# Kernel tuning notes

Measured on AMD Instinct MI355X. Metric: run time of the kernel, lower is better.

Reference implementation:

```python
import jax, jax.numpy as jnp
import numpy as np

N = 50000      # nodes
E = 1600000    # edges (avg degree 32)
R = 32         # num_rels
B = 8          # num_bases
DIN = 128
DOUT = 128


def setup_inputs() -> dict:
    key = jax.random.key(0)
    ks = jax.random.split(key, 7)
    x = jax.random.normal(ks[0], (N, DIN), dtype=jnp.float32)
    src = jax.random.randint(ks[1], (E,), 0, N, dtype=jnp.int32)
    dst = jax.random.randint(ks[2], (E,), 0, N, dtype=jnp.int32)
    etypes = jax.random.randint(ks[3], (E,), 0, R, dtype=jnp.int32)
    weight = jax.random.normal(ks[4], (B, DIN, DOUT), dtype=jnp.float32) * 0.05
    w_comp = jax.random.normal(ks[5], (R, B), dtype=jnp.float32) * 0.3
    h_bias = jnp.zeros((DOUT,), dtype=jnp.float32)
    loop_weight = jax.random.normal(ks[6], (DIN, DOUT), dtype=jnp.float32) * 0.05
    return {"x": x, "src": src, "dst": dst, "etypes": etypes,
            "weight": weight, "w_comp": w_comp, "h_bias": h_bias,
            "loop_weight": loop_weight}


def reference(x, src, dst, etypes, weight, w_comp, h_bias, loop_weight):
    # RelGraphConv, basis regularizer, self_loop=True, bias=True, act=relu, eval (dropout=0).
    # Message m_e = h_{src_e} @ W_{etype_e}, with W_r = sum_b w_comp[r,b] * weight[b].
    # Aggregation is sum over in-edges; since messages are linear in h_src we
    # segment-sum sources into (dst, relation) buckets first, then apply W_r once
    # per node -- identical math, no per-edge [Din,Dout] weight materialization.
    n = x.shape[0]
    r = w_comp.shape[0]
    seg = dst.astype(jnp.int32) * r + etypes.astype(jnp.int32)        # [E]
    agg = jax.ops.segment_sum(x[src], seg, num_segments=n * r)        # [N*R, Din]
    agg = agg.reshape(n, r, -1)                                       # [N, R, Din]
    tmp = jnp.einsum('nri,rb->nbi', agg, w_comp)                      # fold relations into bases
    h = jnp.einsum('nbi,bio->no', tmp, weight)                        # [N, Dout]
    h = h + h_bias + x @ loop_weight                                  # bias + self-loop
    return jax.nn.relu(h)
```

## Files before the change

kernel.cpp:

```cpp
#include <hip/hip_runtime.h>

#define N_NODES 50000
#define N_EDGES 1600000
#define NREL 32
#define NBASES 8
#define DIN 128
#define DOUT 128
#define KTOT (NBASES * DIN)
#define KSL (KTOT + DIN)
#define NODES_PER_BLOCK 8


__global__ void k_hist(const int* __restrict__ dst, int* __restrict__ deg) {
    int e = blockIdx.x * blockDim.x + threadIdx.x;
    if (e < N_EDGES) atomicAdd(&deg[dst[e]], 1);
}

__global__ void k_scan(const int* __restrict__ deg, int* __restrict__ indptr) {
    __shared__ int sdata[1024];
    const int T = 1024;
    int t = threadIdx.x;
    const int chunk = (N_NODES + T - 1) / T;
    int lo = t * chunk;
    int hi = lo + chunk; if (hi > N_NODES) hi = N_NODES;
    if (lo > N_NODES) lo = N_NODES;
    int s = 0;
    for (int i = lo; i < hi; ++i) s += deg[i];
    sdata[t] = s;
    __syncthreads();
    for (int off = 1; off < T; off <<= 1) {
        int v = (t >= off) ? sdata[t - off] : 0;
        __syncthreads();
        sdata[t] += v;
        __syncthreads();
    }
    int base = (t == 0) ? 0 : sdata[t - 1];
    for (int i = lo; i < hi; ++i) { indptr[i] = base; base += deg[i]; }
    if (t == T - 1) indptr[N_NODES] = sdata[T - 1];
}

__global__ void k_scatter(const int* __restrict__ dst,
                          const int* __restrict__ src,
                          const int* __restrict__ ety,
                          const int* __restrict__ indptr,
                          int* __restrict__ cursor,
                          int* __restrict__ packed) {
    int e = blockIdx.x * blockDim.x + threadIdx.x;
    if (e < N_EDGES) {
        int d = dst[e];
        int pos = atomicAdd(&cursor[d], 1);
        packed[indptr[d] + pos] = src[e] | (ety[e] << 16);
    }
}


#define EDGE_FMA(P, XV)                                                      \
    do {                                                                     \
        const float4 wA_ = *(const float4*)&wc[((P) >> 16) * NBASES];        \
        const float4 wB_ = *(const float4*)&wc[((P) >> 16) * NBASES + 4];    \
        a0x += wA_.x * (XV).x; a0y += wA_.x * (XV).y;                        \
        a1x += wA_.y * (XV).x; a1y += wA_.y * (XV).y;                        \
        a2x += wA_.z * (XV).x; a2y += wA_.z * (XV).y;                        \
        a3x += wA_.w * (XV).x; a3y += wA_.w * (XV).y;                        \
        a4x += wB_.x * (XV).x; a4y += wB_.x * (XV).y;                        \
        a5x += wB_.y * (XV).x; a5y += wB_.y * (XV).y;                        \
        a6x += wB_.z * (XV).x; a6y += wB_.z * (XV).y;                        \
        a7x += wB_.w * (XV).x; a7y += wB_.w * (XV).y;                        \
    } while (0)

__launch_bounds__(256, 2)
__global__ void k_fused(const float* __restrict__ x,
                        const float* __restrict__ weight,
                        const float* __restrict__ w_comp,
                        const float* __restrict__ h_bias,
                        const float* __restrict__ loop_w,
                        const int* __restrict__ indptr,
                        const int* __restrict__ packed,
                        float* __restrict__ out) {
    __shared__ __align__(16) float wc[NREL * NBASES];
    __shared__ __align__(16) float tmp[NODES_PER_BLOCK][KSL];

    const int tid  = threadIdx.x;
    const int lane = tid & 63;
    const int wid  = tid >> 6;
    const int nbase = blockIdx.x * NODES_PER_BLOCK;

    wc[tid & 255] = w_comp[tid & 255];
    __syncthreads();

    for (int rep = 0; rep < 2; ++rep) {
        const int nl = wid + rep * 4;
        const int node = nbase + nl;
        float a0x = 0.f, a0y = 0.f, a1x = 0.f, a1y = 0.f;
        float a2x = 0.f, a2y = 0.f, a3x = 0.f, a3y = 0.f;
        float a4x = 0.f, a4y = 0.f, a5x = 0.f, a5y = 0.f;
        float a6x = 0.f, a6y = 0.f, a7x = 0.f, a7y = 0.f;

        *(float2*)&tmp[nl][KTOT + 2 * lane] =
            *(const float2*)&x[(size_t)node * DIN + 2 * lane];

        const int beg = indptr[node], end = indptr[node + 1];
        for (int base = beg; base < end; base += 64) {
            const int cnt = min(64, end - base);
            int pk = 0;
            if (base + lane < end) pk = packed[base + lane];
            int j = 0;
            for (; j + 4 <= cnt; j += 4) {
                const int p0 = __shfl(pk, j + 0);
                const int p1 = __shfl(pk, j + 1);
                const int p2 = __shfl(pk, j + 2);
                const int p3 = __shfl(pk, j + 3);
                const float2 x0 = *(const float2*)&x[(size_t)(p0 & 0xFFFF) * DIN + 2 * lane];
                const float2 x1 = *(const float2*)&x[(size_t)(p1 & 0xFFFF) * DIN + 2 * lane];
                const float2 x2 = *(const float2*)&x[(size_t)(p2 & 0xFFFF) * DIN + 2 * lane];
                const float2 x3 = *(const float2*)&x[(size_t)(p3 & 0xFFFF) * DIN + 2 * lane];
                EDGE_FMA(p0, x0);
                EDGE_FMA(p1, x1);
                EDGE_FMA(p2, x2);
                EDGE_FMA(p3, x3);
            }
            for (; j < cnt; ++j) {
                const int p0 = __shfl(pk, j);
                const float2 x0 = *(const float2*)&x[(size_t)(p0 & 0xFFFF) * DIN + 2 * lane];
                EDGE_FMA(p0, x0);
            }
        }
        *(float2*)&tmp[nl][0 * DIN + 2 * lane] = make_float2(a0x, a0y);
        *(float2*)&tmp[nl][1 * DIN + 2 * lane] = make_float2(a1x, a1y);
        *(float2*)&tmp[nl][2 * DIN + 2 * lane] = make_float2(a2x, a2y);
        *(float2*)&tmp[nl][3 * DIN + 2 * lane] = make_float2(a3x, a3y);
        *(float2*)&tmp[nl][4 * DIN + 2 * lane] = make_float2(a4x, a4y);
        *(float2*)&tmp[nl][5 * DIN + 2 * lane] = make_float2(a5x, a5y);
        *(float2*)&tmp[nl][6 * DIN + 2 * lane] = make_float2(a6x, a6y);
        *(float2*)&tmp[nl][7 * DIN + 2 * lane] = make_float2(a7x, a7y);
    }
    __syncthreads();

    const int d = tid & 127;
    const int half = tid >> 7;
    float o0 = 0.f, o1 = 0.f, o2 = 0.f, o3 = 0.f;

    for (int k = 0; k < KTOT; k += 4) {
        const float wv0 = weight[(k + 0) * DOUT + d];
        const float wv1 = weight[(k + 1) * DOUT + d];
        const float wv2 = weight[(k + 2) * DOUT + d];
        const float wv3 = weight[(k + 3) * DOUT + d];
        const float4 t0 = *(const float4*)&tmp[half + 0][k];
        const float4 t1 = *(const float4*)&tmp[half + 2][k];
        const float4 t2 = *(const float4*)&tmp[half + 4][k];
        const float4 t3 = *(const float4*)&tmp[half + 6][k];
        o0 += t0.x * wv0 + t0.y * wv1 + t0.z * wv2 + t0.w * wv3;
        o1 += t1.x * wv0 + t1.y * wv1 + t1.z * wv2 + t1.w * wv3;
        o2 += t2.x * wv0 + t2.y * wv1 + t2.z * wv2 + t2.w * wv3;
        o3 += t3.x * wv0 + t3.y * wv1 + t3.z * wv2 + t3.w * wv3;
    }
    for (int k = 0; k < DIN; k += 4) {
        const float wv0 = loop_w[(k + 0) * DOUT + d];
        const float wv1 = loop_w[(k + 1) * DOUT + d];
        const float wv2 = loop_w[(k + 2) * DOUT + d];
        const float wv3 = loop_w[(k + 3) * DOUT + d];
        const float4 t0 = *(const float4*)&tmp[half + 0][KTOT + k];
        const float4 t1 = *(const float4*)&tmp[half + 2][KTOT + k];
        const float4 t2 = *(const float4*)&tmp[half + 4][KTOT + k];
        const float4 t3 = *(const float4*)&tmp[half + 6][KTOT + k];
        o0 += t0.x * wv0 + t0.y * wv1 + t0.z * wv2 + t0.w * wv3;
        o1 += t1.x * wv0 + t1.y * wv1 + t1.z * wv2 + t1.w * wv3;
        o2 += t2.x * wv0 + t2.y * wv1 + t2.z * wv2 + t2.w * wv3;
        o3 += t3.x * wv0 + t3.y * wv1 + t3.z * wv2 + t3.w * wv3;
    }

    const float bias = h_bias[d];
    out[(size_t)(nbase + half + 0) * DOUT + d] = fmaxf(o0 + bias, 0.f);
    out[(size_t)(nbase + half + 2) * DOUT + d] = fmaxf(o1 + bias, 0.f);
    out[(size_t)(nbase + half + 4) * DOUT + d] = fmaxf(o2 + bias, 0.f);
    out[(size_t)(nbase + half + 6) * DOUT + d] = fmaxf(o3 + bias, 0.f);
}


extern "C" void kernel_launch(void* const* d_in, const int* in_sizes, int n_in,
                              void* d_out, int out_size, void* d_ws, size_t ws_size,
                              hipStream_t stream) {
    const float* x      = (const float*)d_in[0];
    const int*   src    = (const int*)  d_in[1];
    const int*   dst    = (const int*)  d_in[2];
    const int*   ety    = (const int*)  d_in[3];
    const float* weight = (const float*)d_in[4];
    const float* w_comp = (const float*)d_in[5];
    const float* h_bias = (const float*)d_in[6];
    const float* loop_w = (const float*)d_in[7];
    float* out = (float*)d_out;

    int* deg    = (int*)d_ws;
    int* indptr = deg + N_NODES;
    int* cursor = indptr + N_NODES + 1;
    int* packed = cursor + N_NODES;

    hipMemsetAsync(d_ws, 0, (size_t)(3 * N_NODES + 1) * sizeof(int), stream);

    k_hist<<<(N_EDGES + 255) / 256, 256, 0, stream>>>(dst, deg);
    k_scan<<<1, 1024, 0, stream>>>(deg, indptr);
    k_scatter<<<(N_EDGES + 255) / 256, 256, 0, stream>>>(dst, src, ety, indptr, cursor, packed);
    k_fused<<<N_NODES / NODES_PER_BLOCK, 256, 0, stream>>>(
        x, weight, w_comp, h_bias, loop_w, indptr, packed, out);
}
```

Before: 751.7 us.

## Store basis activations and transposed weights in bf16, double nodes per block

```diff
diff --git a/kernel.cpp b/kernel.cpp
--- a/kernel.cpp
+++ b/kernel.cpp
@@ -7,8 +7,18 @@
 #define DIN 128
 #define DOUT 128
 #define KTOT (NBASES * DIN)
-#define KSL (KTOT + DIN)
-#define NODES_PER_BLOCK 8
+#define KSL  (KTOT + DIN)
+#define KPAD 1160
+#define NPB  16
+
+typedef __attribute__((ext_vector_type(8))) short short8;
+typedef __attribute__((ext_vector_type(4))) float f32x4;
+
+static __device__ __forceinline__ ushort f2bf(float f) {
+    uint u = __float_as_uint(f);
+    u += 0x7FFF + ((u >> 16) & 1);
+    return (ushort)(u >> 16);
+}
 
 
 __global__ void k_hist(const int* __restrict__ dst, int* __restrict__ deg) {
@@ -53,6 +63,16 @@
     }
 }
 
+__global__ void k_wconv(const float* __restrict__ weight,
+                        const float* __restrict__ loop_w,
+                        ushort* __restrict__ wbT) {
+    const int e = blockIdx.x * blockDim.x + threadIdx.x;
+    const int k = e >> 7;
+    const int n = e & 127;
+    const float v = (k < KTOT) ? weight[e] : loop_w[e - KTOT * DIN];
+    wbT[n * KSL + k] = f2bf(v);
+}
+
 
 #define EDGE_FMA(P, XV)                                                      \
     do {                                                                     \
@@ -68,36 +88,47 @@
         a7x += wB_.w * (XV).x; a7y += wB_.w * (XV).y;                        \
     } while (0)
 
+#define ROWACC(J, OJ)                                                        \
+    {                                                                        \
+        const uint2 tp = *(const uint2*)&tmp16[half + 2 * (J)][k];           \
+        OJ += __uint_as_float(tp.x << 16) * w0                               \
+            + __uint_as_float(tp.x & 0xFFFF0000u) * w1                       \
+            + __uint_as_float(tp.y << 16) * w2                               \
+            + __uint_as_float(tp.y & 0xFFFF0000u) * w3;                      \
+    }
+
 __launch_bounds__(256, 2)
 __global__ void k_fused(const float* __restrict__ x,
-                        const float* __restrict__ weight,
                         const float* __restrict__ w_comp,
                         const float* __restrict__ h_bias,
-                        const float* __restrict__ loop_w,
                         const int* __restrict__ indptr,
                         const int* __restrict__ packed,
+                        const ushort* __restrict__ wbT,
                         float* __restrict__ out) {
-    __shared__ __align__(16) float wc[NREL * NBASES];
-    __shared__ __align__(16) float tmp[NODES_PER_BLOCK][KSL];
+    __shared__ float wc[NREL * NBASES];
+    __shared__ __align__(16) ushort tmp16[NPB][KPAD];
 
     const int tid  = threadIdx.x;
     const int lane = tid & 63;
     const int wid  = tid >> 6;
-    const int nbase = blockIdx.x * NODES_PER_BLOCK;
-
-    wc[tid & 255] = w_comp[tid & 255];
+    const int nbase = blockIdx.x * NPB;
+
+    wc[tid] = w_comp[tid];
     __syncthreads();
 
-    for (int rep = 0; rep < 2; ++rep) {
-        const int nl = wid + rep * 4;
+    for (int rep = 0; rep < 4; ++rep) {
+        const int nl = rep * 4 + wid;
         const int node = nbase + nl;
         float a0x = 0.f, a0y = 0.f, a1x = 0.f, a1y = 0.f;
         float a2x = 0.f, a2y = 0.f, a3x = 0.f, a3y = 0.f;
         float a4x = 0.f, a4y = 0.f, a5x = 0.f, a5y = 0.f;
         float a6x = 0.f, a6y = 0.f, a7x = 0.f, a7y = 0.f;
 
-        *(float2*)&tmp[nl][KTOT + 2 * lane] =
-            *(const float2*)&x[(size_t)node * DIN + 2 * lane];
+        {
+            const float2 xs = *(const float2*)&x[(size_t)node * DIN + 2 * lane];
+            *(uint*)&tmp16[nl][KTOT + 2 * lane] =
+                (uint)f2bf(xs.x) | ((uint)f2bf(xs.y) << 16);
+        }
 
         const int beg = indptr[node], end = indptr[node + 1];
         for (int base = beg; base < end; base += 64) {
@@ -125,55 +156,42 @@
                 EDGE_FMA(p0, x0);
             }
         }
-        *(float2*)&tmp[nl][0 * DIN + 2 * lane] = make_float2(a0x, a0y);
-        *(float2*)&tmp[nl][1 * DIN + 2 * lane] = make_float2(a1x, a1y);
-        *(float2*)&tmp[nl][2 * DIN + 2 * lane] = make_float2(a2x, a2y);
-        *(float2*)&tmp[nl][3 * DIN + 2 * lane] = make_float2(a3x, a3y);
-        *(float2*)&tmp[nl][4 * DIN + 2 * lane] = make_float2(a4x, a4y);
-        *(float2*)&tmp[nl][5 * DIN + 2 * lane] = make_float2(a5x, a5y);
-        *(float2*)&tmp[nl][6 * DIN + 2 * lane] = make_float2(a6x, a6y);
-        *(float2*)&tmp[nl][7 * DIN + 2 * lane] = make_float2(a7x, a7y);
+        *(uint*)&tmp16[nl][0 * DIN + 2 * lane] = (uint)f2bf(a0x) | ((uint)f2bf(a0y) << 16);
+        *(uint*)&tmp16[nl][1 * DIN + 2 * lane] = (uint)f2bf(a1x) | ((uint)f2bf(a1y) << 16);
+        *(uint*)&tmp16[nl][2 * DIN + 2 * lane] = (uint)f2bf(a2x) | ((uint)f2bf(a2y) << 16);
+        *(uint*)&tmp16[nl][3 * DIN + 2 * lane] = (uint)f2bf(a3x) | ((uint)f2bf(a3y) << 16);
+        *(uint*)&tmp16[nl][4 * DIN + 2 * lane] = (uint)f2bf(a4x) | ((uint)f2bf(a4y) << 16);
+        *(uint*)&tmp16[nl][5 * DIN + 2 * lane] = (uint)f2bf(a5x) | ((uint)f2bf(a5y) << 16);
+        *(uint*)&tmp16[nl][6 * DIN + 2 * lane] = (uint)f2bf(a6x) | ((uint)f2bf(a6y) << 16);
+        *(uint*)&tmp16[nl][7 * DIN + 2 * lane] = (uint)f2bf(a7x) | ((uint)f2bf(a7y) << 16);
     }
     __syncthreads();
 
     const int d = tid & 127;
     const int half = tid >> 7;
     float o0 = 0.f, o1 = 0.f, o2 = 0.f, o3 = 0.f;
-
-    for (int k = 0; k < KTOT; k += 4) {
-        const float wv0 = weight[(k + 0) * DOUT + d];
-        const float wv1 = weight[(k + 1) * DOUT + d];
-        const float wv2 = weight[(k + 2) * DOUT + d];
-        const float wv3 = weight[(k + 3) * DOUT + d];
-        const float4 t0 = *(const float4*)&tmp[half + 0][k];
-        const float4 t1 = *(const float4*)&tmp[half + 2][k];
-        const float4 t2 = *(const float4*)&tmp[half + 4][k];
-        const float4 t3 = *(const float4*)&tmp[half + 6][k];
-        o0 += t0.x * wv0 + t0.y * wv1 + t0.z * wv2 + t0.w * wv3;
-        o1 += t1.x * wv0 + t1.y * wv1 + t1.z * wv2 + t1.w * wv3;
-        o2 += t2.x * wv0 + t2.y * wv1 + t2.z * wv2 + t2.w * wv3;
-        o3 += t3.x * wv0 + t3.y * wv1 + t3.z * wv2 + t3.w * wv3;
-    }
-    for (int k = 0; k < DIN; k += 4) {
-        const float wv0 = loop_w[(k + 0) * DOUT + d];
-        const float wv1 = loop_w[(k + 1) * DOUT + d];
-        const float wv2 = loop_w[(k + 2) * DOUT + d];
-        const float wv3 = loop_w[(k + 3) * DOUT + d];
-        const float4 t0 = *(const float4*)&tmp[half + 0][KTOT + k];
-        const float4 t1 = *(const float4*)&tmp[half + 2][KTOT + k];
-        const float4 t2 = *(const float4*)&tmp[half + 4][KTOT + k];
-        const float4 t3 = *(const float4*)&tmp[half + 6][KTOT + k];
-        o0 += t0.x * wv0 + t0.y * wv1 + t0.z * wv2 + t0.w * wv3;
-        o1 += t1.x * wv0 + t1.y * wv1 + t1.z * wv2 + t1.w * wv3;
-        o2 += t2.x * wv0 + t2.y * wv1 + t2.z * wv2 + t2.w * wv3;
-        o3 += t3.x * wv0 + t3.y * wv1 + t3.z * wv2 + t3.w * wv3;
+    float o4 = 0.f, o5 = 0.f, o6 = 0.f, o7 = 0.f;
+
+    const ushort* wrow = &wbT[(size_t)d * KSL];
+    for (int k = 0; k < KSL; k += 4) {
+        const uint2 wp = *(const uint2*)(wrow + k);
+        const float w0 = __uint_as_float(wp.x << 16);
+        const float w1 = __uint_as_float(wp.x & 0xFFFF0000u);
+        const float w2 = __uint_as_float(wp.y << 16);
+        const float w3 = __uint_as_float(wp.y & 0xFFFF0000u);
+        ROWACC(0, o0); ROWACC(1, o1); ROWACC(2, o2); ROWACC(3, o3);
+        ROWACC(4, o4); ROWACC(5, o5); ROWACC(6, o6); ROWACC(7, o7);
     }
 
     const float bias = h_bias[d];
-    out[(size_t)(nbase + half + 0) * DOUT + d] = fmaxf(o0 + bias, 0.f);
-    out[(size_t)(nbase + half + 2) * DOUT + d] = fmaxf(o1 + bias, 0.f);
-    out[(size_t)(nbase + half + 4) * DOUT + d] = fmaxf(o2 + bias, 0.f);
-    out[(size_t)(nbase + half + 6) * DOUT + d] = fmaxf(o3 + bias, 0.f);
+    out[(size_t)(nbase + half +  0) * DOUT + d] = fmaxf(o0 + bias, 0.f);
+    out[(size_t)(nbase + half +  2) * DOUT + d] = fmaxf(o1 + bias, 0.f);
+    out[(size_t)(nbase + half +  4) * DOUT + d] = fmaxf(o2 + bias, 0.f);
+    out[(size_t)(nbase + half +  6) * DOUT + d] = fmaxf(o3 + bias, 0.f);
+    out[(size_t)(nbase + half +  8) * DOUT + d] = fmaxf(o4 + bias, 0.f);
+    out[(size_t)(nbase + half + 10) * DOUT + d] = fmaxf(o5 + bias, 0.f);
+    out[(size_t)(nbase + half + 12) * DOUT + d] = fmaxf(o6 + bias, 0.f);
+    out[(size_t)(nbase + half + 14) * DOUT + d] = fmaxf(o7 + bias, 0.f);
 }
 
 
@@ -194,12 +212,15 @@
     int* indptr = deg + N_NODES;
     int* cursor = indptr + N_NODES + 1;
     int* packed = cursor + N_NODES;
+    const size_t woff = ((size_t)(3 * N_NODES + 1 + N_EDGES) + 15) & ~(size_t)15;
+    ushort* wbT = (ushort*)((int*)d_ws + woff);
 
     hipMemsetAsync(d_ws, 0, (size_t)(3 * N_NODES + 1) * sizeof(int), stream);
 
+    k_wconv<<<(DOUT * KSL) / 256, 256, 0, stream>>>(weight, loop_w, wbT);
     k_hist<<<(N_EDGES + 255) / 256, 256, 0, stream>>>(dst, deg);
     k_scan<<<1, 1024, 0, stream>>>(deg, indptr);
     k_scatter<<<(N_EDGES + 255) / 256, 256, 0, stream>>>(dst, src, ety, indptr, cursor, packed);
-    k_fused<<<N_NODES / NODES_PER_BLOCK, 256, 0, stream>>>(
-        x, weight, w_comp, h_bias, loop_w, indptr, packed, out);
-}
+    k_fused<<<N_NODES / NPB, 256, 0, stream>>>(
+        x, w_comp, h_bias, indptr, packed, wbT, out);
+}
```

Result: slower. 909.8 us (+21.0%).
